# Performance work log

Hardware: AMD Instinct MI355X
Metric: run time of the kernel (lower is better)

The kernel has to match this reference:

```python
import jax, jax.numpy as jnp
import numpy as np

B = 512          # batch_size
C = 4            # num_classes
N = 16384        # grid unknowns per sample (128x128)
H = 0.0078125    # grid spacing h = 1/128


def setup_inputs() -> dict:
    key = jax.random.key(0)
    k1, k2, k3 = jax.random.split(key, 3)
    coefficients = jax.random.uniform(k1, (B, N), dtype=jnp.float32)  # positive -> A SPD
    predictions = jax.random.normal(k2, (B, C, N), dtype=jnp.float32)
    targets = jax.random.normal(k3, (B, N, C), dtype=jnp.float32)
    return {"coefficients": coefficients, "predictions": predictions, "targets": targets}


def reference(coefficients, predictions, targets):
    # A = diag(h^2 * coefficients[i]); exploit diagonality: A @ v == a * v.
    a = (H * H) * coefficients                      # [B, N] diagonal of A per sample
    preds = predictions.reshape(B, C, -1)           # predictions.view(batch_size, num_classes, -1)

    # Modified Gram-Schmidt in the A-inner product, vectorized over batch.
    ortho = []
    for j in range(C):                              # tiny fixed loop over classes
        v = preds[:, j, :]                          # [B, N]
        for e in ortho:
            proj = jnp.sum(v * (a * e), axis=-1, keepdims=True)  # <v, A e>
            v = v - proj * e
        n2 = jnp.sum(v * a * v, axis=-1, keepdims=True)          # <v, A v>
        safe = jnp.where(n2 > 0, n2, jnp.float32(1.0))
        v = jnp.where(n2 > 0, v * jax.lax.rsqrt(safe), v)        # normalize iff <v,Av> > 0
        ortho.append(v)
    Cm = jnp.stack(ortho, axis=1)                   # [B, C, N]

    # M = C_i @ A @ targets[i] for each sample -> [B, C, C]
    M = jnp.einsum('bcn,bnm->bcm', Cm * a[:, None, :], targets)
    per_sample = (jnp.float32(4.0) - jnp.sum(M * M, axis=(1, 2))) / jnp.float32(4.0)
    return jnp.mean(per_sample)
```

## Files before the change

### kernel.cpp

```cpp
#include <hip/hip_runtime.h>

#define BSZ 512
#define NC  4
#define NN  16384
#define H2  (0.0078125f * 0.0078125f)

#define BLK   256
#define SSEG  4
#define NG    (NN / 4)
#define GSEG  (NG / SSEG)
#define ITERS (GSEG / BLK)

__device__ __forceinline__ void accum_elem(float c,
                                           float p0, float p1, float p2, float p3,
                                           float tx, float ty, float tz, float tw,
                                           float* acc)
{
    float cp0 = c * p0, cp1 = c * p1, cp2 = c * p2, cp3 = c * p3;
    acc[0]  += cp0 * p0;  acc[1]  += cp0 * p1;  acc[2]  += cp0 * p2;  acc[3]  += cp0 * p3;
    acc[4]  += cp1 * p1;  acc[5]  += cp1 * p2;  acc[6]  += cp1 * p3;
    acc[7]  += cp2 * p2;  acc[8]  += cp2 * p3;
    acc[9]  += cp3 * p3;
    acc[10] += cp0 * tx;  acc[11] += cp0 * ty;  acc[12] += cp0 * tz;  acc[13] += cp0 * tw;
    acc[14] += cp1 * tx;  acc[15] += cp1 * ty;  acc[16] += cp1 * tz;  acc[17] += cp1 * tw;
    acc[18] += cp2 * tx;  acc[19] += cp2 * ty;  acc[20] += cp2 * tz;  acc[21] += cp2 * tw;
    acc[22] += cp3 * tx;  acc[23] += cp3 * ty;  acc[24] += cp3 * tz;  acc[25] += cp3 * tw;
}

__global__ __launch_bounds__(BLK, 2)
void loss_partial(const float* __restrict__ coef,
                  const float* __restrict__ pred,
                  const float* __restrict__ targ,
                  float* __restrict__ ws)
{
    const int seg = blockIdx.x;
    const int b   = blockIdx.y;
    const int tid = threadIdx.x;

    const float4* __restrict__ c4 = (const float4*)(coef + (size_t)b * NN);
    const float4* __restrict__ q0 = (const float4*)(pred + (size_t)b * NC * NN + 0 * NN);
    const float4* __restrict__ q1 = (const float4*)(pred + (size_t)b * NC * NN + 1 * NN);
    const float4* __restrict__ q2 = (const float4*)(pred + (size_t)b * NC * NN + 2 * NN);
    const float4* __restrict__ q3 = (const float4*)(pred + (size_t)b * NC * NN + 3 * NN);
    const float4* __restrict__ t4 = (const float4*)(targ + (size_t)b * NN * NC);

    float acc[26];
#pragma unroll
    for (int k = 0; k < 26; ++k) acc[k] = 0.f;

#pragma unroll 1
    for (int it = 0; it < ITERS; ++it) {
        const int g = seg * GSEG + it * BLK + tid;
        float4 cc = c4[g];
        float4 a0 = q0[g];
        float4 a1 = q1[g];
        float4 a2 = q2[g];
        float4 a3 = q3[g];
        float4 t0 = t4[4 * g + 0];
        float4 t1 = t4[4 * g + 1];
        float4 t2 = t4[4 * g + 2];
        float4 t3 = t4[4 * g + 3];

        accum_elem(cc.x, a0.x, a1.x, a2.x, a3.x, t0.x, t0.y, t0.z, t0.w, acc);
        accum_elem(cc.y, a0.y, a1.y, a2.y, a3.y, t1.x, t1.y, t1.z, t1.w, acc);
        accum_elem(cc.z, a0.z, a1.z, a2.z, a3.z, t2.x, t2.y, t2.z, t2.w, acc);
        accum_elem(cc.w, a0.w, a1.w, a2.w, a3.w, t3.x, t3.y, t3.z, t3.w, acc);
    }

    const int lane = tid & 63;
    const int wv   = tid >> 6;
    __shared__ float red[26][4];

#pragma unroll
    for (int k = 0; k < 26; ++k) {
        float v = acc[k];
#pragma unroll
        for (int o = 32; o > 0; o >>= 1) v += __shfl_down(v, o, 64);
        if (lane == 0) red[k][wv] = v;
    }
    __syncthreads();

    if (tid < 26) {
        float v = red[tid][0] + red[tid][1] + red[tid][2] + red[tid][3];
        ws[((size_t)seg * 26 + tid) * BSZ + b] = v;
    }
}

__global__ __launch_bounds__(BSZ)
void finalize(const float* __restrict__ ws, float* __restrict__ out)
{
    const int b = threadIdx.x;

    float s[26];
#pragma unroll
    for (int k = 0; k < 26; ++k) s[k] = 0.f;
#pragma unroll
    for (int seg = 0; seg < SSEG; ++seg)
#pragma unroll
        for (int k = 0; k < 26; ++k)
            s[k] += ws[((size_t)seg * 26 + k) * BSZ + b];
#pragma unroll
    for (int k = 0; k < 26; ++k) s[k] *= H2;

    float Gm[4][4];
    Gm[0][0] = s[0];
    Gm[0][1] = Gm[1][0] = s[1];
    Gm[0][2] = Gm[2][0] = s[2];
    Gm[0][3] = Gm[3][0] = s[3];
    Gm[1][1] = s[4];
    Gm[1][2] = Gm[2][1] = s[5];
    Gm[1][3] = Gm[3][1] = s[6];
    Gm[2][2] = s[7];
    Gm[2][3] = Gm[3][2] = s[8];
    Gm[3][3] = s[9];

    float Tm[4][4];
#pragma unroll
    for (int i = 0; i < 4; ++i)
#pragma unroll
        for (int m = 0; m < 4; ++m) Tm[i][m] = s[10 + 4 * i + m];

    float u[4][4];
#pragma unroll
    for (int j = 0; j < 4; ++j) {
        float w[4];
#pragma unroll
        for (int i = 0; i < 4; ++i) w[i] = (i == j) ? 1.f : 0.f;
#pragma unroll
        for (int k = 0; k < 4; ++k) {
            if (k < j) {
                float proj = 0.f;
#pragma unroll
                for (int i = 0; i < 4; ++i) {
                    float gu = 0.f;
#pragma unroll
                    for (int l = 0; l < 4; ++l) gu += Gm[i][l] * u[k][l];
                    proj += w[i] * gu;
                }
#pragma unroll
                for (int i = 0; i < 4; ++i) w[i] -= proj * u[k][i];
            }
        }
        float n2 = 0.f;
#pragma unroll
        for (int i = 0; i < 4; ++i) {
            float gw = 0.f;
#pragma unroll
            for (int l = 0; l < 4; ++l) gw += Gm[i][l] * w[l];
            n2 += w[i] * gw;
        }
        float sc = (n2 > 0.f) ? rsqrtf(n2) : 1.f;
#pragma unroll
        for (int i = 0; i < 4; ++i) u[j][i] = w[i] * sc;
    }

    float ssum = 0.f;
#pragma unroll
    for (int c = 0; c < 4; ++c) {
#pragma unroll
        for (int m = 0; m < 4; ++m) {
            float M = 0.f;
#pragma unroll
            for (int i = 0; i < 4; ++i) M += u[c][i] * Tm[i][m];
            ssum += M * M;
        }
    }
    float ps = (4.f - ssum) * 0.25f;

#pragma unroll
    for (int o = 32; o > 0; o >>= 1) ps += __shfl_down(ps, o, 64);
    __shared__ float red[8];
    if ((b & 63) == 0) red[b >> 6] = ps;
    __syncthreads();
    if (b == 0) {
        float t = 0.f;
#pragma unroll
        for (int w = 0; w < 8; ++w) t += red[w];
        out[0] = t / (float)BSZ;
    }
}

extern "C" void kernel_launch(void* const* d_in, const int* in_sizes, int n_in,
                              void* d_out, int out_size, void* d_ws, size_t ws_size,
                              hipStream_t stream)
{
    const float* coef = (const float*)d_in[0];
    const float* pred = (const float*)d_in[1];
    const float* targ = (const float*)d_in[2];
    float* out = (float*)d_out;
    float* ws  = (float*)d_ws;

    dim3 grid(SSEG, BSZ);
    loss_partial<<<grid, BLK, 0, stream>>>(coef, pred, targ, ws);
    finalize<<<1, BSZ, 0, stream>>>(ws, out);
}
```

Before: 304.6 us.

## Double-buffer tiles through LDS with async global_load_lds DMA

Replaces direct per-thread float4 global loads with a two-stage LDS pipeline. Each tile of 1024 elements (coefficients, four prediction rows and interleaved targets) is copied global-to-LDS with 16-byte global_load_lds, and the next tile is fetched while the current one is accumulated. The aim is to hide memory latency in a loop that was previously serialized on its loads and running well below bandwidth. It uses 72KB of LDS per block, which limits occupancy. Correctness depends on the DMA being complete before the barrier that precedes compute.

```diff
diff --git a/kernel.cpp b/kernel.cpp
--- a/kernel.cpp
+++ b/kernel.cpp
@@ -1,4 +1,5 @@
 #include <hip/hip_runtime.h>
+#include <stdint.h>
 
 #define BSZ 512
 #define NC  4
@@ -7,24 +8,16 @@
 
 #define BLK   256
 #define SSEG  4
-#define NG    (NN / 4)
-#define GSEG  (NG / SSEG)
-#define ITERS (GSEG / BLK)
-
-__device__ __forceinline__ void accum_elem(float c,
-                                           float p0, float p1, float p2, float p3,
-                                           float tx, float ty, float tz, float tw,
-                                           float* acc)
-{
-    float cp0 = c * p0, cp1 = c * p1, cp2 = c * p2, cp3 = c * p3;
-    acc[0]  += cp0 * p0;  acc[1]  += cp0 * p1;  acc[2]  += cp0 * p2;  acc[3]  += cp0 * p3;
-    acc[4]  += cp1 * p1;  acc[5]  += cp1 * p2;  acc[6]  += cp1 * p3;
-    acc[7]  += cp2 * p2;  acc[8]  += cp2 * p3;
-    acc[9]  += cp3 * p3;
-    acc[10] += cp0 * tx;  acc[11] += cp0 * ty;  acc[12] += cp0 * tz;  acc[13] += cp0 * tw;
-    acc[14] += cp1 * tx;  acc[15] += cp1 * ty;  acc[16] += cp1 * tz;  acc[17] += cp1 * tw;
-    acc[18] += cp2 * tx;  acc[19] += cp2 * ty;  acc[20] += cp2 * tz;  acc[21] += cp2 * tw;
-    acc[22] += cp3 * tx;  acc[23] += cp3 * ty;  acc[24] += cp3 * tz;  acc[25] += cp3 * tw;
+#define TILE  1024
+#define TPB   (NN / SSEG / TILE)
+#define BUF_F (TILE + NC * TILE + NC * TILE)
+
+__device__ __forceinline__ void dma16(const float* g, float* l)
+{
+    __builtin_amdgcn_global_load_lds(
+        (const __attribute__((address_space(1))) uint32_t*)g,
+        (__attribute__((address_space(3))) uint32_t*)l,
+        16, 0, 0);
 }
 
 __global__ __launch_bounds__(BLK, 2)
@@ -37,34 +30,71 @@
     const int b   = blockIdx.y;
     const int tid = threadIdx.x;
 
-    const float4* __restrict__ c4 = (const float4*)(coef + (size_t)b * NN);
-    const float4* __restrict__ q0 = (const float4*)(pred + (size_t)b * NC * NN + 0 * NN);
-    const float4* __restrict__ q1 = (const float4*)(pred + (size_t)b * NC * NN + 1 * NN);
-    const float4* __restrict__ q2 = (const float4*)(pred + (size_t)b * NC * NN + 2 * NN);
-    const float4* __restrict__ q3 = (const float4*)(pred + (size_t)b * NC * NN + 3 * NN);
-    const float4* __restrict__ t4 = (const float4*)(targ + (size_t)b * NN * NC);
+    const float* __restrict__ cb = coef + (size_t)b * NN;
+    const float* __restrict__ pb = pred + (size_t)b * NC * NN;
+    const float* __restrict__ tg = targ + (size_t)b * NN * NC;
+
+    const int segbase = seg * (NN / SSEG);
+
+    __shared__ float buf[2][BUF_F];
 
     float acc[26];
 #pragma unroll
     for (int k = 0; k < 26; ++k) acc[k] = 0.f;
 
+    auto stage = [&](int t, int q) {
+        const int E = segbase + t * TILE;
+        float* bc = &buf[q][0];
+        float* bp = &buf[q][TILE];
+        float* bt = &buf[q][TILE + NC * TILE];
+        dma16(cb + E + tid * 4, bc + tid * 4);
+#pragma unroll
+        for (int j = 0; j < NC; ++j)
+            dma16(pb + (size_t)j * NN + E + tid * 4, bp + j * TILE + tid * 4);
+#pragma unroll
+        for (int i = 0; i < 4; ++i) {
+            const int c = i * BLK + tid;
+            dma16(tg + (size_t)E * NC + c * 4, bt + c * 4);
+        }
+    };
+
+    auto compute = [&](int q) {
+        const float* bc = &buf[q][0];
+        const float* bp = &buf[q][TILE];
+        const float* bt = &buf[q][TILE + NC * TILE];
+#pragma unroll
+        for (int u = 0; u < TILE / BLK; ++u) {
+            const int e = u * BLK + tid;
+            float c  = bc[e];
+            float p0 = bp[0 * TILE + e];
+            float p1 = bp[1 * TILE + e];
+            float p2 = bp[2 * TILE + e];
+            float p3 = bp[3 * TILE + e];
+            float4 tv = ((const float4*)bt)[e];
+            float cp0 = c * p0, cp1 = c * p1, cp2 = c * p2, cp3 = c * p3;
+            acc[0]  += cp0 * p0;  acc[1]  += cp0 * p1;
+            acc[2]  += cp0 * p2;  acc[3]  += cp0 * p3;
+            acc[4]  += cp1 * p1;  acc[5]  += cp1 * p2;
+            acc[6]  += cp1 * p3;
+            acc[7]  += cp2 * p2;  acc[8]  += cp2 * p3;
+            acc[9]  += cp3 * p3;
+            acc[10] += cp0 * tv.x; acc[11] += cp0 * tv.y;
+            acc[12] += cp0 * tv.z; acc[13] += cp0 * tv.w;
+            acc[14] += cp1 * tv.x; acc[15] += cp1 * tv.y;
+            acc[16] += cp1 * tv.z; acc[17] += cp1 * tv.w;
+            acc[18] += cp2 * tv.x; acc[19] += cp2 * tv.y;
+            acc[20] += cp2 * tv.z; acc[21] += cp2 * tv.w;
+            acc[22] += cp3 * tv.x; acc[23] += cp3 * tv.y;
+            acc[24] += cp3 * tv.z; acc[25] += cp3 * tv.w;
+        }
+    };
+
+    stage(0, 0);
 #pragma unroll 1
-    for (int it = 0; it < ITERS; ++it) {
-        const int g = seg * GSEG + it * BLK + tid;
-        float4 cc = c4[g];
-        float4 a0 = q0[g];
-        float4 a1 = q1[g];
-        float4 a2 = q2[g];
-        float4 a3 = q3[g];
-        float4 t0 = t4[4 * g + 0];
-        float4 t1 = t4[4 * g + 1];
-        float4 t2 = t4[4 * g + 2];
-        float4 t3 = t4[4 * g + 3];
-
-        accum_elem(cc.x, a0.x, a1.x, a2.x, a3.x, t0.x, t0.y, t0.z, t0.w, acc);
-        accum_elem(cc.y, a0.y, a1.y, a2.y, a3.y, t1.x, t1.y, t1.z, t1.w, acc);
-        accum_elem(cc.z, a0.z, a1.z, a2.z, a3.z, t2.x, t2.y, t2.z, t2.w, acc);
-        accum_elem(cc.w, a0.w, a1.w, a2.w, a3.w, t3.x, t3.y, t3.z, t3.w, acc);
+    for (int t = 0; t < TPB; ++t) {
+        __syncthreads();
+        if (t + 1 < TPB) stage(t + 1, (t + 1) & 1);
+        compute(t & 1);
     }
 
     const int lane = tid & 63;
```

Result: no change. 304.1 us (-0.2%).
